# Kernel tuning notes

Measured on AMD Instinct MI355X. Metric: run time of the kernel, lower is better.

Reference implementation:

```python
import jax, jax.numpy as jnp
import numpy as np
from jax import lax

T, B = 32, 16
NUM_ACTIONS = 18
HID = 256
C_V, C_K, C_S, NQ = 120, 8, 64, 4
NKEY, NVAL = C_K + C_S, C_V + C_S
Hh, Ww = 27, 20


def _spatial_basis():
    # Fourier spatial basis from Mott et al.; U = V = 8 -> 64 channels.
    h, w, U = Hh, Ww, 8
    p_h = np.arange(1, h + 1)[:, None] * np.ones((1, w)) * (np.pi / h)
    p_w = np.ones((h, 1)) * np.arange(1, w + 1)[None, :] * (np.pi / w)
    u = np.arange(1, U + 1)
    a = np.cos(p_h[:, :, None] * u)  # (h,w,8)
    b = np.cos(p_w[:, :, None] * u)  # (h,w,8)
    S = np.einsum('hwu,hwv->hwuv', a, b).reshape(h, w, U * U)
    return jnp.asarray(S, jnp.float32)

_S = _spatial_basis()


def _conv(x, w, b, stride, pad):
    y = lax.conv_general_dilated(x, w, stride, pad,
                                 dimension_numbers=('NCHW', 'OIHW', 'NCHW'))
    return y + b[None, :, None, None]


def setup_inputs() -> dict:
    key = jax.random.key(0)
    ks = iter(jax.random.split(key, 40))
    f32 = jnp.float32
    def rn(shape, s=0.05):
        return jax.random.normal(next(ks), shape, dtype=f32) * s
    return dict(
        frame=jax.random.normal(next(ks), (T, B, 3, 210, 160), dtype=f32),
        done=jnp.zeros((T, B), dtype=bool),
        last_action=jax.random.randint(next(ks), (T, B), 0, NUM_ACTIONS),
        reward=jax.random.normal(next(ks), (T, B), dtype=f32),
        core_h=jnp.zeros((B, HID), f32), core_c=jnp.zeros((B, HID), f32),
        conv_h=jnp.zeros((B, HID // 2, Hh, Ww), f32),
        conv_c=jnp.zeros((B, HID // 2, Hh, Ww), f32),
        cnn_w1=rn((32, 3, 8, 8)), cnn_b1=rn((32,)),
        cnn_w2=rn((64, 32, 4, 4)), cnn_b2=rn((64,)),
        lstm_w=rn((512, 192, 3, 3)), lstm_b=rn((512,)),
        qw1=rn((HID, 128)), qb1=rn((128,)),
        qw2=rn((128, NQ * NKEY)), qb2=rn((NQ * NKEY,)),
        qw3=rn((NQ * NKEY, NQ * NKEY)), qb3=rn((NQ * NKEY,)),
        aw1=rn((NVAL * NQ + NKEY * NQ + 1 + NUM_ACTIONS, 2 * HID)), ab1=rn((2 * HID,)),
        aw2=rn((2 * HID, HID)), ab2=rn((HID,)),
        w_ih=rn((4 * HID, HID)), w_hh=rn((4 * HID, HID)),
        b_ih=rn((4 * HID,)), b_hh=rn((4 * HID,)),
        pw=rn((HID, NUM_ACTIONS)), pb=rn((NUM_ACTIONS,)),
        vw=rn((HID, 1)), vb=rn((1,)),
    )


def reference(frame, done, last_action, reward, core_h, core_c, conv_h, conv_c,
              cnn_w1, cnn_b1, cnn_w2, cnn_b2, lstm_w, lstm_b,
              qw1, qb1, qw2, qb2, qw3, qb3, aw1, ab1, aw2, ab2,
              w_ih, w_hh, b_ih, b_hh, pw, pb, vw, vb):
    x = frame.reshape(T * B, 3, 210, 160)
    x = _conv(x, cnn_w1, cnn_b1, (4, 4), [(1, 1), (2, 2)])
    x = _conv(x, cnn_w2, cnn_b2, (2, 2), [(2, 2), (1, 1)])  # (T*B,64,27,20)
    x = x.reshape(T, B, 64, Hh, Ww)
    nd = (~done).astype(jnp.float32)  # (T,B)

    def vis_step(carry, inp):
        h, c = carry
        x_t, nd_t = inp
        m = nd_t[:, None, None, None]
        h, c = m * h, m * c
        gates = _conv(jnp.concatenate([x_t, h], axis=1), lstm_w, lstm_b,
                      (1, 1), [(1, 1), (1, 1)])
        ai, af, ao, ag = jnp.split(gates, 4, axis=1)
        c = jax.nn.sigmoid(af) * c + jax.nn.sigmoid(ai) * jnp.tanh(ag)
        h = jax.nn.sigmoid(ao) * jnp.tanh(c)
        return (h, c), h

    (vh, vc), O = lax.scan(vis_step, (conv_h, conv_c), (x, nd))
    # Faithful to the original `.view(N, h, w, c)` (a reinterpret, not a transpose).
    O = O.reshape(T * B, Hh, Ww, 128)
    Sb = jnp.broadcast_to(_S, (T * B, Hh, Ww, C_S))
    K = jnp.concatenate([O[..., :C_K], Sb], axis=3).reshape(T, B, Hh, Ww, NKEY)
    V = jnp.concatenate([O[..., C_K:], Sb], axis=3).reshape(T, B, Hh, Ww, NVAL)

    a1h = jax.nn.one_hot(last_action, NUM_ACTIONS, dtype=jnp.float32)  # (T,B,A)
    r = jnp.clip(reward, -1.0, 1.0)[..., None]  # (T,B,1)

    def core_step(carry, inp):
        h, c = carry
        K_t, V_t, r_t, a_t, nd_t = inp
        q = jax.nn.relu(h @ qw1 + qb1)
        q = jax.nn.relu(q @ qw2 + qb2)
        q = (q @ qw3 + qb3).reshape(B, NQ, NKEY)
        A = jnp.einsum('bhwk,bqk->bhwq', K_t, q)
        A = jax.nn.softmax(A.reshape(B, Hh * Ww, NQ), axis=1).reshape(B, Hh, Ww, NQ)
        ans = jnp.einsum('bhwq,bhwv->bqv', A, V_t)  # (B,NQ,NVAL)
        answer = jnp.concatenate(
            [ans.reshape(B, -1), q.reshape(B, -1), r_t, a_t], axis=1)
        ci = jax.nn.relu(answer @ aw1 + ab1) @ aw2 + ab2
        m = nd_t[:, None]
        h, c = m * h, m * c
        gates = ci @ w_ih.T + b_ih + h @ w_hh.T + b_hh  # torch gate order i,f,g,o
        gi, gf, gg, go = jnp.split(gates, 4, axis=1)
        c = jax.nn.sigmoid(gf) * c + jax.nn.sigmoid(gi) * jnp.tanh(gg)
        h = jax.nn.sigmoid(go) * jnp.tanh(c)
        return (h, c), h

    (ch, cc), outs = lax.scan(core_step, (core_h, core_c), (K, V, r, a1h, nd))
    out = outs.reshape(T * B, HID)
    logits = out @ pw + pb
    values = out @ vw + vb
    action = jnp.argmax(logits, axis=1)  # eval-mode action selection
    return (logits.reshape(T, B, NUM_ACTIONS), values.reshape(T, B),
            action.reshape(T, B), ch, cc, vh, vc)
```

## Files before the change

### kernel.cpp

```cpp
#include <hip/hip_runtime.h>
#include <math.h>

#define T_ 32
#define B_ 16
#define NA 18
#define P_ 540

typedef __attribute__((ext_vector_type(8)))  short short8;
typedef __attribute__((ext_vector_type(16))) float f32x16;

__device__ __forceinline__ float sigm(float x){ return 1.0f/(1.0f+expf(-x)); }
__device__ __forceinline__ unsigned short f2bf(float f){
    unsigned u = __float_as_uint(f);
    u += 0x7fff + ((u>>16)&1u);
    return (unsigned short)(u>>16);
}
__device__ __forceinline__ float bfu(unsigned short u){ return __uint_as_float(((unsigned)u)<<16); }
__device__ __forceinline__ float BFLO(unsigned x){ return __uint_as_float(x<<16); }
__device__ __forceinline__ float BFHI(unsigned x){ return __uint_as_float(x & 0xffff0000u); }

__device__ __forceinline__ void conv1_block(const float* __restrict__ frame,
                                            const float* __restrict__ w,
                                            const float* __restrict__ bias,
                                            unsigned short* __restrict__ c1buf,
                                            int n, int slot, int oh, int tid, char* smraw){
    float* tile = (float*)smraw;
    const float* fb = frame + (size_t)n*3*210*160;
    for (int s = tid; s < 6048; s += 512){
        int col = s % 168;
        int row = (s/168) % 12;
        int ic  = s / 2016;
        int iy = oh*4 - 1 + row;
        int ix = col - 2;
        float v = 0.f;
        if (iy >= 0 && iy < 210 && ix >= 0 && ix < 160) v = fb[ic*33600 + iy*160 + ix];
        tile[s] = v;
    }
    __syncthreads();
    int oc = tid & 31, grp = (tid >> 5) & 7, rsel = tid >> 8;
    float acc[5] = {0.f,0.f,0.f,0.f,0.f};
    const float* wb = w + oc*192;
    for (int ic=0; ic<3; ++ic){
        #pragma unroll
        for (int kh=0; kh<8; ++kh){
            const float* wr = wb + ic*64 + kh*8;
            float4 w0 = *((const float4*)wr);
            float4 w1 = *((const float4*)(wr+4));
            const float* row = tile + ic*2016 + (kh + 4*rsel)*168 + grp*20;
            float r[24];
            *((float4*)(r+ 0)) = *((const float4*)(row+ 0));
            *((float4*)(r+ 4)) = *((const float4*)(row+ 4));
            *((float4*)(r+ 8)) = *((const float4*)(row+ 8));
            *((float4*)(r+12)) = *((const float4*)(row+12));
            *((float4*)(r+16)) = *((const float4*)(row+16));
            *((float4*)(r+20)) = *((const float4*)(row+20));
            #pragma unroll
            for (int o=0;o<5;++o){
                acc[o] += r[o*4+0]*w0.x + r[o*4+1]*w0.y + r[o*4+2]*w0.z + r[o*4+3]*w0.w
                        + r[o*4+4]*w1.x + r[o*4+5]*w1.y + r[o*4+6]*w1.z + r[o*4+7]*w1.w;
            }
        }
    }
    float bi = bias[oc];
    unsigned short* ob = c1buf + ((size_t)((slot*16 + (n & 15))*32 + oc)*56 + oh+2+rsel)*42 + 1;
    #pragma unroll
    for (int o=0;o<5;++o) ob[grp*5+o] = f2bf(acc[o] + bi);
}

__device__ __forceinline__ void c2_block(const unsigned short* __restrict__ c1buf,
                                         const unsigned short* __restrict__ apack2,
                                         const float* __restrict__ bias,
                                         unsigned short* __restrict__ xre,
                                         int s, int slot, int n0, int tid, char* smraw){
    unsigned short (*p2)[3072] = (unsigned short (*)[3072])smraw;
    float* bsm = (float*)(smraw + 12288);
    int wave = tid >> 6, lane = tid & 63;
    int khalf = (lane>>5) << 3;
    if (tid < 64) bsm[tid] = bias[tid];
    const unsigned short* cb = c1buf + (size_t)(slot*16 + (s & 15))*32*2352;

    int soff[4], swaddr[4];
    #pragma unroll
    for (int q=0;q<4;++q){
        int idx = q*512 + tid;
        int n = idx & 127, k = idx >> 7;
        int p = n0 + n; if (p > 539) p = 539;
        soff[q] = ((p/20)*2 + (k>>2))*42 + (p%20)*2 + (k&3);
        swaddr[q] = n*24 + k;
    }
    #pragma unroll
    for (int q=0;q<4;++q) p2[0][swaddr[q]] = cb[soff[q]];
    unsigned short rv[4];
    #pragma unroll
    for (int q=0;q<4;++q) rv[q] = cb[2352 + soff[q]];

    int mt = wave >> 2, nq = wave & 3;
    short8 acur = *((const short8*)(apack2 + ((size_t)mt*64 + lane)*8));
    short8 anxt;
    f32x16 acc;
    #pragma unroll
    for (int rg=0;rg<16;++rg) acc[rg] = 0.f;
    __syncthreads();

    for (int c=0; c<32; ++c){
        int buf = c & 1;
        if (c < 31){
            #pragma unroll
            for (int q=0;q<4;++q) p2[buf^1][swaddr[q]] = rv[q];
        }
        if (c < 30){
            const unsigned short* src = cb + (size_t)(c+2)*2352;
            #pragma unroll
            for (int q=0;q<4;++q) rv[q] = src[soff[q]];
        }
        if (c < 31) anxt = *((const short8*)(apack2 + ((size_t)((c+1)*2 + mt)*64 + lane)*8));
        {
            int n = nq*32 + (lane & 31);
            short8 bf = *((const short8*)(&p2[buf][n*24 + khalf]));
            acc = __builtin_amdgcn_mfma_f32_32x32x16_bf16(acur, bf, acc, 0, 0, 0);
        }
        acur = anxt;
        __syncthreads();
    }
    int pos = n0 + nq*32 + (lane & 31);
    if (pos < 540){
        unsigned short* op = xre + ((size_t)s*540 + pos)*64;
        #pragma unroll
        for (int rg=0; rg<16; ++rg){
            int oc = mt*32 + (rg & 3) + 8*(rg>>2) + 4*(lane>>5);
            op[oc] = f2bf(acc[rg] + bsm[oc]);
        }
    }
}

__global__ __launch_bounds__(512) void conv1pro(const float* __restrict__ frame,
                                                const float* __restrict__ w,
                                                const float* __restrict__ bias,
                                                unsigned short* __restrict__ c1buf){
    __shared__ __align__(16) char sm[24576];
    int n = blockIdx.x/26, oh = (blockIdx.x%26)*2;
    conv1_block(frame, w, bias, c1buf, n, (n>>4)%3, oh, threadIdx.x, sm);
}
__global__ __launch_bounds__(512) void c2pro(const unsigned short* __restrict__ c1buf,
                                             const unsigned short* __restrict__ apack2,
                                             const float* __restrict__ bias,
                                             unsigned short* __restrict__ xre){
    __shared__ __align__(16) char sm[12544];
    c2_block(c1buf, apack2, bias, xre, blockIdx.x/5, 0, (blockIdx.x%5)*128, threadIdx.x, sm);
}

__global__ void apack2k(const float* __restrict__ w2, unsigned short* __restrict__ ap){
    int idx = blockIdx.x*256 + threadIdx.x;
    if (idx >= 32768) return;
    int j = idx & 7;
    int lane = (idx>>3) & 63;
    int mt = (idx>>9) & 1;
    int ic = idx >> 10;
    int k = ((lane>>5)<<3) + j;
    int oc = mt*32 + (lane & 31);
    ap[idx] = f2bf(w2[((oc*32 + ic)<<4) + k]);
}

__global__ void sbasisk(float* __restrict__ S, float* __restrict__ ST){
    int idx = blockIdx.x*256 + threadIdx.x;
    if (idx >= P_*64) return;
    int s = idx & 63, p = idx >> 6;
    int y = p/20, x = p%20;
    int u = s >> 3, v = s & 7;
    double a  = cos((double)((y+1)*(u+1)) * M_PI / 27.0);
    double bb = cos((double)((x+1)*(v+1)) * M_PI / 20.0);
    float fv = (float)(a*bb);
    S[idx] = fv;
    ST[(size_t)s*540 + p] = fv;
}

__global__ void packw8k(const float* __restrict__ in, unsigned short* __restrict__ out, int R, int C){
    int idx = blockIdx.x*256 + threadIdx.x;
    int r8cnt = (R+7)>>3;
    if (idx >= r8cnt*C*8) return;
    int j = idx & 7;
    int rc = idx >> 3;
    int c = rc % C;
    int r = (rc / C)*8 + j;
    out[idx] = (r < R) ? f2bf(in[(size_t)r*C + c]) : (unsigned short)0;
}
__global__ void packt8k(const float* __restrict__ in, unsigned short* __restrict__ out, int R, int C){
    int idx = blockIdx.x*256 + threadIdx.x;
    int r8cnt = (R+7)>>3;
    if (idx >= r8cnt*C*8) return;
    int j = idx & 7;
    int rc = idx >> 3;
    int c = rc % C;
    int r = (rc / C)*8 + j;
    out[idx] = (r < R) ? f2bf(in[(size_t)c*R + r]) : (unsigned short)0;
}

__global__ void apack9k(const float* __restrict__ lw, unsigned short* __restrict__ ap){
    int idx = blockIdx.x*256 + threadIdx.x;
    if (idx >= 884736) return;
    int j = idx & 7;
    int lane = (idx>>3) & 63;
    int mt = (idx>>9) & 15;
    int f  = idx >> 13;
    int tap = f / 12, c = f % 12;
    int ch = c*16 + ((lane>>5)<<3) + j;
    int oc = mt*32 + (lane & 31);
    ap[idx] = f2bf(lw[(size_t)oc*1728 + ch*9 + tap]);
}

__global__ void h0rek(const float* __restrict__ h0, unsigned short* __restrict__ h0re){
    int idx = blockIdx.x*256 + threadIdx.x;
    if (idx >= 16*128*540) return;
    int plane = idx / 540, p = idx % 540;
    int b = plane >> 7, c = plane & 127;
    h0re[((size_t)b*540 + p)*128 + c] = f2bf(h0[idx]);
}

__global__ __launch_bounds__(512) void gvck(const float* __restrict__ frame,
                                            const float* __restrict__ cnn_w1,
                                            const float* __restrict__ cnn_b1,
                                            unsigned short* __restrict__ c1buf,
                                            const unsigned short* __restrict__ apack2,
                                            const float* __restrict__ cnn_b2,
                                            unsigned short* __restrict__ xre,
                                            const unsigned short* __restrict__ hrd,
                                            unsigned short* __restrict__ hwr,
                                            const unsigned short* __restrict__ h0re,
                                            const unsigned short* __restrict__ apack,
                                            const float* __restrict__ lb,
                                            const unsigned char* __restrict__ done,
                                            float* __restrict__ vh, float* __restrict__ vc,
                                            unsigned short* __restrict__ hreA,
                                            const float* __restrict__ S,
                                            const float* __restrict__ ST,
                                            const unsigned short* __restrict__ pq1, const float* __restrict__ qb1,
                                            const unsigned short* __restrict__ pq2, const float* __restrict__ qb2,
                                            const unsigned short* __restrict__ pq3, const float* __restrict__ qb3,
                                            const unsigned short* __restrict__ pa1, const float* __restrict__ ab1,
                                            const unsigned short* __restrict__ pa2, const float* __restrict__ ab2,
                                            const unsigned short* __restrict__ pih, const unsigned short* __restrict__ phh,
                                            const float* __restrict__ bih, const float* __restrict__ bhh,
                                            const float* __restrict__ reward, const int* __restrict__ lact,
                                            float* __restrict__ hsb, float* __restrict__ csb,
                                            float* __restrict__ outs,
                                            int t){
    __shared__ __align__(16) char smraw[65536];
    int bid = blockIdx.x;
    int tid = threadIdx.x;

    if (bid >= 720){
        int tp1 = t + 1; if (tp1 > 31) return;
        int idx = bid - 720;
        c2_block(c1buf, apack2, cnn_b2, xre, tp1*16 + idx/5, tp1%3, (idx%5)*128, tid, smraw);
        return;
    }
    if (bid >= 304){
        int tp2 = t + 2; if (tp2 > 31) return;
        int idx = bid - 304;
        conv1_block(frame, cnn_w1, cnn_b1, c1buf, tp2*16 + idx/26, tp2%3, (idx%26)*2, tid, smraw);
        return;
    }

    if (bid >= 16){
        if (t >= T_) return;
        float* gsm = (float*)smraw;
        int vb = bid - 16;
        int b  = vb % 16;
        int r  = vb / 16;
        int nb = r % 9;
        int mh = r / 9;
        int wave = tid >> 6, lane = tid & 63;
        int khalf = (lane>>5) << 3;
        int n0 = nb * 64;
        bool dn = done[t*B_ + b];

        const unsigned short* xb = xre + (size_t)(t*B_ + b)*540*64;
        const unsigned short* hp2 = (t==0) ? (h0re + (size_t)b*540*128)
                                           : (hrd  + (size_t)b*540*128);

        int mt = (wave>>1)*4 + mh*2 + (wave&1);

        int poff[2][9]; int vmask[2][9];
        #pragma unroll
        for (int jj=0;jj<2;++jj){
            int p = n0 + jj*32 + (lane & 31); if (p > 539) p = 539;
            int y = p/20, x = p%20;
            #pragma unroll
            for (int tap=0;tap<9;++tap){
                int dy = tap/3 - 1, dx = tap%3 - 1;
                int yy = y+dy, xx = x+dx;
                vmask[jj][tap] = ((unsigned)yy < 27u) && ((unsigned)xx < 20u);
                poff[jj][tap] = yy*20 + xx;
            }
        }
        const short8 z8 = {0,0,0,0,0,0,0,0};
        f32x16 acc[2];
        #pragma unroll
        for (int jj=0;jj<2;++jj)
            #pragma unroll
            for (int rg=0;rg<16;++rg) acc[jj][rg] = 0.f;

        for (int c=0;c<4;++c){
            int cho = c*16 + khalf;
            #pragma unroll
            for (int tap=0;tap<9;++tap){
                short8 af = *((const short8*)(apack + ((size_t)((tap*12+c)*16 + mt)*64 + lane)*8));
                short8 b0 = vmask[0][tap] ? *((const short8*)(xb + poff[0][tap]*64 + cho)) : z8;
                short8 b1 = vmask[1][tap] ? *((const short8*)(xb + poff[1][tap]*64 + cho)) : z8;
                acc[0] = __builtin_amdgcn_mfma_f32_32x32x16_bf16(af, b0, acc[0], 0, 0, 0);
                acc[1] = __builtin_amdgcn_mfma_f32_32x32x16_bf16(af, b1, acc[1], 0, 0, 0);
            }
        }
        if (!dn){
            for (int c=4;c<12;++c){
                int cho = (c-4)*16 + khalf;
                #pragma unroll
                for (int tap=0;tap<9;++tap){
                    short8 af = *((const short8*)(apack + ((size_t)((tap*12+c)*16 + mt)*64 + lane)*8));
                    short8 b0 = vmask[0][tap] ? *((const short8*)(hp2 + poff[0][tap]*128 + cho)) : z8;
                    short8 b1 = vmask[1][tap] ? *((const short8*)(hp2 + poff[1][tap]*128 + cho)) : z8;
                    acc[0] = __builtin_amdgcn_mfma_f32_32x32x16_bf16(af, b0, acc[0], 0, 0, 0);
                    acc[1] = __builtin_amdgcn_mfma_f32_32x32x16_bf16(af, b1, acc[1], 0, 0, 0);
                }
            }
        }

        int g8 = wave >> 1, ih = wave & 1;
        #pragma unroll
        for (int j=0;j<2;++j){
            int p_loc = j*32 + (lane & 31);
            #pragma unroll
            for (int rg=0; rg<16; ++rg){
                int c_loc = ih*32 + 4*(lane>>5) + (rg & 3) + 8*(rg>>2);
                gsm[g8*4096 + c_loc*64 + p_loc] = acc[j][rg];
            }
        }
        __syncthreads();

        {
            int p_loc = tid & 63, c0 = tid >> 6;
            int pg = n0 + p_loc;
            if (pg < 540){
                float m = dn ? 0.f : 1.f;
                #pragma unroll
                for (int e=0;e<8;++e){
                    int c_loc = c0*8 + e;
                    int cg = mh*64 + c_loc;
                    float gi = gsm[        c_loc*64 + p_loc] + lb[      cg];
                    float gf = gsm[ 4096 + c_loc*64 + p_loc] + lb[128 + cg];
                    float go = gsm[ 8192 + c_loc*64 + p_loc] + lb[256 + cg];
                    float gg = gsm[12288 + c_loc*64 + p_loc] + lb[384 + cg];
                    size_t idx = ((size_t)b*128 + cg)*540 + pg;
                    float cold = vc[idx] * m;
                    float cn = sigm(gf)*cold + sigm(gi)*tanhf(gg);
                    float hn = sigm(go)*tanhf(cn);
                    vc[idx] = cn;
                    if (t == T_-1) vh[idx] = hn;
                    unsigned short hb16 = f2bf(hn);
                    hwr[((size_t)b*540 + pg)*128 + cg] = hb16;
                    int flat = cg*540 + pg;
                    int pos = (flat/2560)*20 + (flat/128)%20;
                    int ch  = flat & 127;
                    hreA[((size_t)(t*B_ + b)*540 + pos)*128 + ch] = hb16;
                }
            }
        }
        return;
    }

    if (t == 0) return;
    int tc = t - 1;
    int b = bid;
    float* fs = (float*)smraw;
    float* hs   = fs;
    float* cs   = fs + 256;
    float* hs2  = fs + 512;
    float* q1   = fs + 768;
    float* q2   = fs + 896;
    float* q3   = fs + 1184;
    float* elog = fs + 1472;
    float* red  = fs + 3632;
    float* ansv = fs + 3664;
    float* hid  = fs + 4720;
    float* cis  = fs + 5232;
    float* gb   = fs + 5488;

    if (tid < 256){ hs[tid] = hsb[b*256+tid]; cs[tid] = csb[b*256+tid]; }
    if (tid >= 256 && tid < 269) ansv[1043 + (tid-256)] = 0.f;
    __syncthreads();

    float m = done[tc*B_+b] ? 0.f : 1.f;
    if (tid < 128){
        float a0=0.f,a1=0.f,a2=0.f,a3=0.f;
        for (int i8=0;i8<32;++i8){
            uint4 w = *((const uint4*)(pq1 + ((size_t)(i8<<7)+tid)*8));
            float4 ha = *((const float4*)(hs + i8*8));
            float4 hb2 = *((const float4*)(hs + i8*8 + 4));
            a0 += ha.x*BFLO(w.x);  a1 += ha.y*BFHI(w.x);
            a2 += ha.z*BFLO(w.y);  a3 += ha.w*BFHI(w.y);
            a0 += hb2.x*BFLO(w.z); a1 += hb2.y*BFHI(w.z);
            a2 += hb2.z*BFLO(w.w); a3 += hb2.w*BFHI(w.w);
        }
        q1[tid] = fmaxf(qb1[tid] + ((a0+a1)+(a2+a3)), 0.f);
    }
    __syncthreads();
    if (tid < 288){
        float a0=0.f,a1=0.f,a2=0.f,a3=0.f;
        for (int i8=0;i8<16;++i8){
            uint4 w = *((const uint4*)(pq2 + ((size_t)i8*288+tid)*8));
            float4 ha = *((const float4*)(q1 + i8*8));
            float4 hb2 = *((const float4*)(q1 + i8*8 + 4));
            a0 += ha.x*BFLO(w.x);  a1 += ha.y*BFHI(w.x);
            a2 += ha.z*BFLO(w.y);  a3 += ha.w*BFHI(w.y);
            a0 += hb2.x*BFLO(w.z); a1 += hb2.y*BFHI(w.z);
            a2 += hb2.z*BFLO(w.w); a3 += hb2.w*BFHI(w.w);
        }
        q2[tid] = fmaxf(qb2[tid] + ((a0+a1)+(a2+a3)), 0.f);
    }
    __syncthreads();
    if (tid < 288){
        float a0=0.f,a1=0.f,a2=0.f,a3=0.f;
        for (int i8=0;i8<36;++i8){
            uint4 w = *((const uint4*)(pq3 + ((size_t)i8*288+tid)*8));
            float4 ha = *((const float4*)(q2 + i8*8));
            float4 hb2 = *((const float4*)(q2 + i8*8 + 4));
            a0 += ha.x*BFLO(w.x);  a1 += ha.y*BFHI(w.x);
            a2 += ha.z*BFLO(w.y);  a3 += ha.w*BFHI(w.y);
            a0 += hb2.x*BFLO(w.z); a1 += hb2.y*BFHI(w.z);
            a2 += hb2.z*BFLO(w.w); a3 += hb2.w*BFHI(w.w);
        }
        float a = qb3[tid] + ((a0+a1)+(a2+a3));
        q3[tid] = a;
        ansv[736+tid] = a;
    }
    if (tid == 0){ float r = reward[tc*B_+b]; ansv[1024] = fminf(1.f,fmaxf(-1.f,r)); }
    if (tid >= 32 && tid < 32+NA) ansv[1025 + tid-32] = (lact[tc*B_+b] == tid-32) ? 1.f : 0.f;
    __syncthreads();

    const unsigned short* hrb = hreA + (size_t)(tc*B_ + b)*540*128;
    for (int idx = tid; idx < 4*P_; idx += 512){
        int qi = idx / P_, p = idx % P_;
        const unsigned short* hp = hrb + (size_t)p*128;
        uint4 hv = *((const uint4*)hp);
        const float* qv = q3 + qi*72;
        float a = BFLO(hv.x)*qv[0] + BFHI(hv.x)*qv[1]
                + BFLO(hv.y)*qv[2] + BFHI(hv.y)*qv[3]
                + BFLO(hv.z)*qv[4] + BFHI(hv.z)*qv[5]
                + BFLO(hv.w)*qv[6] + BFHI(hv.w)*qv[7];
        const float* Sp = S + p*64;
        #pragma unroll
        for (int s2=0;s2<16;++s2){
            float4 sv = *((const float4*)(Sp + 4*s2));
            a += sv.x*qv[8+4*s2] + sv.y*qv[9+4*s2] + sv.z*qv[10+4*s2] + sv.w*qv[11+4*s2];
        }
        elog[qi*P_ + p] = a;
    }
    __syncthreads();
    {
        int qi = tid >> 7, lt = tid & 127;
        float mx = -1e30f;
        for (int p = lt; p < P_; p += 128) mx = fmaxf(mx, elog[qi*P_ + p]);
        for (int off=32; off; off>>=1) mx = fmaxf(mx, __shfl_down(mx, off));
        if ((tid & 63) == 0) red[tid>>6] = mx;
        __syncthreads();
        if (tid < 4) red[16+tid] = fmaxf(red[2*tid], red[2*tid+1]);
        __syncthreads();
        mx = red[16+qi];
        float sm = 0.f;
        for (int p = lt; p < P_; p += 128){ float e = expf(elog[qi*P_ + p]-mx); elog[qi*P_ + p] = e; sm += e; }
        for (int off=32; off; off>>=1) sm += __shfl_down(sm, off);
        if ((tid & 63) == 0) red[8 + (tid>>6)] = sm;
        __syncthreads();
        if (tid < 4) red[24+tid] = red[8+2*tid] + red[8+2*tid+1];
        __syncthreads();
    }
    if (tid < 480){
        int g = tid >> 3;
        int qi = g / 15, vb = g % 15;
        int pc = tid & 7;
        float ac[8] = {0,0,0,0,0,0,0,0};
        const unsigned short* hb8 = hrb + 8 + vb*8;
        for (int p = pc; p < P_; p += 8){
            float e = elog[qi*P_ + p];
            uint4 hv = *((const uint4*)(hb8 + (size_t)p*128));
            ac[0] += e*BFLO(hv.x); ac[1] += e*BFHI(hv.x);
            ac[2] += e*BFLO(hv.y); ac[3] += e*BFHI(hv.y);
            ac[4] += e*BFLO(hv.z); ac[5] += e*BFHI(hv.z);
            ac[6] += e*BFLO(hv.w); ac[7] += e*BFHI(hv.w);
        }
        #pragma unroll
        for (int j=0;j<8;++j){ ac[j] += __shfl_down(ac[j],4); ac[j] += __shfl_down(ac[j],2); ac[j] += __shfl_down(ac[j],1); }
        if (pc == 0){
            float inv2 = 1.f/red[24+qi];
            #pragma unroll
            for (int j=0;j<8;++j) ansv[qi*184 + vb*8 + j] = ac[j]*inv2;
        }
    }
    {
        int g = tid >> 3;
        int qi = g >> 4, vb4 = g & 15;
        int pc = tid & 7;
        float s0=0.f, s1=0.f, s2v=0.f, s3=0.f;
        const float* S0 = ST + (size_t)(vb4*4)*540;
        for (int p = pc; p < P_; p += 8){
            float e = elog[qi*P_ + p];
            s0 += e*S0[p]; s1 += e*S0[540+p]; s2v += e*S0[1080+p]; s3 += e*S0[1620+p];
        }
        s0 += __shfl_down(s0,4); s0 += __shfl_down(s0,2); s0 += __shfl_down(s0,1);
        s1 += __shfl_down(s1,4); s1 += __shfl_down(s1,2); s1 += __shfl_down(s1,1);
        s2v += __shfl_down(s2v,4); s2v += __shfl_down(s2v,2); s2v += __shfl_down(s2v,1);
        s3 += __shfl_down(s3,4); s3 += __shfl_down(s3,2); s3 += __shfl_down(s3,1);
        if (pc == 0){
            float inv2 = 1.f/red[24+qi];
            ansv[qi*184 + 120 + vb4*4 + 0] = s0*inv2;
            ansv[qi*184 + 120 + vb4*4 + 1] = s1*inv2;
            ansv[qi*184 + 120 + vb4*4 + 2] = s2v*inv2;
            ansv[qi*184 + 120 + vb4*4 + 3] = s3*inv2;
        }
    }
    __syncthreads();
    {
        float a0=ab1[tid], a1=0.f, a2=0.f, a3=0.f;
        for (int i8=0;i8<131;++i8){
            uint4 w = *((const uint4*)(pa1 + ((size_t)(i8<<9)+tid)*8));
            float4 av = *((const float4*)(ansv + i8*8));
            float4 av2 = *((const float4*)(ansv + i8*8 + 4));
            a0 += av.x*BFLO(w.x);  a1 += av.y*BFHI(w.x);
            a2 += av.z*BFLO(w.y);  a3 += av.w*BFHI(w.y);
            a0 += av2.x*BFLO(w.z); a1 += av2.y*BFHI(w.z);
            a2 += av2.z*BFLO(w.w); a3 += av2.w*BFHI(w.w);
        }
        hid[tid] = fmaxf((a0+a1)+(a2+a3), 0.f);
    }
    if (tid < 256) hs2[tid] = hs[tid]*m;
    __syncthreads();
    if (tid < 256){
        float a0=ab2[tid],a1=0.f,a2=0.f,a3=0.f;
        for (int i8=0;i8<64;++i8){
            uint4 w = *((const uint4*)(pa2 + ((size_t)(i8<<8)+tid)*8));
            float4 hv = *((const float4*)(hid + i8*8));
            float4 hv2 = *((const float4*)(hid + i8*8 + 4));
            a0 += hv.x*BFLO(w.x);  a1 += hv.y*BFHI(w.x);
            a2 += hv.z*BFLO(w.y);  a3 += hv.w*BFHI(w.y);
            a0 += hv2.x*BFLO(w.z); a1 += hv2.y*BFHI(w.z);
            a2 += hv2.z*BFLO(w.w); a3 += hv2.w*BFHI(w.w);
        }
        cis[tid] = (a0+a1)+(a2+a3);
    }
    __syncthreads();
    for (int g = tid; g < 1024; g += 512){
        float a0=bih[g]+bhh[g], a1=0.f, a2=0.f, a3=0.f;
        for (int i8=0;i8<32;++i8){
            uint4 wi = *((const uint4*)(pih + ((size_t)(i8<<10)+g)*8));
            uint4 wh = *((const uint4*)(phh + ((size_t)(i8<<10)+g)*8));
            float4 ca = *((const float4*)(cis + i8*8));
            float4 cb2 = *((const float4*)(cis + i8*8 + 4));
            float4 ha = *((const float4*)(hs2 + i8*8));
            float4 hb2 = *((const float4*)(hs2 + i8*8 + 4));
            a0 += ca.x*BFLO(wi.x) + ha.x*BFLO(wh.x);
            a1 += ca.y*BFHI(wi.x) + ha.y*BFHI(wh.x);
            a2 += ca.z*BFLO(wi.y) + ha.z*BFLO(wh.y);
            a3 += ca.w*BFHI(wi.y) + ha.w*BFHI(wh.y);
            a0 += cb2.x*BFLO(wi.z) + hb2.x*BFLO(wh.z);
            a1 += cb2.y*BFHI(wi.z) + hb2.y*BFHI(wh.z);
            a2 += cb2.z*BFLO(wi.w) + hb2.z*BFLO(wh.w);
            a3 += cb2.w*BFHI(wi.w) + hb2.w*BFHI(wh.w);
        }
        gb[g] = (a0+a1)+(a2+a3);
    }
    __syncthreads();
    if (tid < 256){
        float gi = gb[tid], gf = gb[256+tid], gg = gb[512+tid], go = gb[768+tid];
        float cold = cs[tid]*m;
        float cn = sigm(gf)*cold + sigm(gi)*tanhf(gg);
        float hn = sigm(go)*tanhf(cn);
        csb[b*256+tid] = cn;
        hsb[b*256+tid] = hn;
        outs[(tc*B_+b)*256+tid] = hn;
    }
}

__global__ __launch_bounds__(64) void finalk(const float* __restrict__ outs,
                                             const float* __restrict__ pw, const float* __restrict__ pb,
                                             const float* __restrict__ vw, const float* __restrict__ vb,
                                             float* __restrict__ dout){
    int row = blockIdx.x, tid = threadIdx.x;
    __shared__ float os[256];
    __shared__ float lg[NA];
    for (int i=tid; i<256; i+=64) os[i] = outs[row*256+i];
    __syncthreads();
    if (tid < NA){
        float a = pb[tid];
        for (int i=0;i<256;++i) a += os[i]*pw[i*NA+tid];
        lg[tid] = a;
        dout[row*NA + tid] = a;
    } else if (tid == 32){
        float a = vb[0];
        for (int i=0;i<256;++i) a += os[i]*vw[i];
        dout[9216 + row] = a;
    }
    __syncthreads();
    if (tid == 0){
        int am = 0; float bv = lg[0];
        for (int j=1;j<NA;++j) if (lg[j] > bv){ bv = lg[j]; am = j; }
        dout[9728 + row] = (float)am;
    }
}

extern "C" void kernel_launch(void* const* d_in, const int* in_sizes, int n_in,
                              void* d_out, int out_size, void* d_ws, size_t ws_size,
                              hipStream_t stream) {
    const float* frame   = (const float*)d_in[0];
    const unsigned char* done = (const unsigned char*)d_in[1];
    const int*   lact    = (const int*)d_in[2];
    const float* reward  = (const float*)d_in[3];
    const float* core_h0 = (const float*)d_in[4];
    const float* core_c0 = (const float*)d_in[5];
    const float* conv_h0 = (const float*)d_in[6];
    const float* conv_c0 = (const float*)d_in[7];
    const float* cnn_w1  = (const float*)d_in[8];
    const float* cnn_b1  = (const float*)d_in[9];
    const float* cnn_w2  = (const float*)d_in[10];
    const float* cnn_b2  = (const float*)d_in[11];
    const float* lstm_w  = (const float*)d_in[12];
    const float* lstm_b  = (const float*)d_in[13];
    const float* qw1 = (const float*)d_in[14]; const float* qb1 = (const float*)d_in[15];
    const float* qw2 = (const float*)d_in[16]; const float* qb2 = (const float*)d_in[17];
    const float* qw3 = (const float*)d_in[18]; const float* qb3 = (const float*)d_in[19];
    const float* aw1 = (const float*)d_in[20]; const float* ab1 = (const float*)d_in[21];
    const float* aw2 = (const float*)d_in[22]; const float* ab2 = (const float*)d_in[23];
    const float* w_ih = (const float*)d_in[24]; const float* w_hh = (const float*)d_in[25];
    const float* b_ih = (const float*)d_in[26]; const float* b_hh = (const float*)d_in[27];
    const float* pw = (const float*)d_in[28]; const float* pb = (const float*)d_in[29];
    const float* vw = (const float*)d_in[30]; const float* vb = (const float*)d_in[31];

    float* ws = (float*)d_ws;
    float* dout = (float*)d_out;

    unsigned short* xre    = (unsigned short*)ws;
    unsigned short* hreA   = (unsigned short*)(ws + 10485760);
    unsigned short* apack  = (unsigned short*)(ws + 28180480);
    unsigned short* wpk    = (unsigned short*)(ws + 28966912);
    unsigned short* pq1 = wpk;
    unsigned short* pq2 = wpk + 32768;
    unsigned short* pq3 = wpk + 69632;
    unsigned short* pa1 = wpk + 152576;
    unsigned short* pa2 = wpk + 689152;
    unsigned short* pih = wpk + 820224;
    unsigned short* phh = wpk + 1082368;
    unsigned short* h0re   = (unsigned short*)(ws + 29753344);
    unsigned short* apack2 = (unsigned short*)(ws + 30408704);
    unsigned short* hpl0   = (unsigned short*)(ws + 30425088);
    float* hsb   = ws + 31080448;
    float* csb   = ws + 31084544;
    unsigned short* hpl1   = (unsigned short*)(ws + 31100928);
    unsigned short* c1buf  = (unsigned short*)(ws + 31653888);
    float* ST    = ws + 33460224;
    float* vh    = ws + 34881536;
    float* vc    = ws + 35987456;
    float* S     = ws + 37093376;
    float* outs  = ws + 37127936;

    hipMemsetAsync(c1buf, 0, (size_t)3612672*2, stream);

    apack2k<<<128, 256, 0, stream>>>(cnn_w2, apack2);
    sbasisk<<<135, 256, 0, stream>>>(S, ST);
    apack9k<<<3456, 256, 0, stream>>>(lstm_w, apack);
    packw8k<<<128,  256, 0, stream>>>(qw1, pq1, 256, 128);
    packw8k<<<144,  256, 0, stream>>>(qw2, pq2, 128, 288);
    packw8k<<<324,  256, 0, stream>>>(qw3, pq3, 288, 288);
    packw8k<<<2096, 256, 0, stream>>>(aw1, pa1, 1043, 512);
    packw8k<<<512,  256, 0, stream>>>(aw2, pa2, 512, 256);
    packt8k<<<1024, 256, 0, stream>>>(w_ih, pih, 256, 1024);
    packt8k<<<1024, 256, 0, stream>>>(w_hh, phh, 256, 1024);
    h0rek<<<4320, 256, 0, stream>>>(conv_h0, h0re);
    hipMemcpyAsync(vc,  conv_c0, (size_t)16*128*540*sizeof(float), hipMemcpyDeviceToDevice, stream);
    hipMemcpyAsync(hsb, core_h0, (size_t)16*256*sizeof(float), hipMemcpyDeviceToDevice, stream);
    hipMemcpyAsync(csb, core_c0, (size_t)16*256*sizeof(float), hipMemcpyDeviceToDevice, stream);

    conv1pro<<<832, 512, 0, stream>>>(frame, cnn_w1, cnn_b1, c1buf);
    c2pro<<<80, 512, 0, stream>>>(c1buf, apack2, cnn_b2, xre);

    for (int t = 0; t <= T_; ++t){
        gvck<<<800, 512, 0, stream>>>(frame, cnn_w1, cnn_b1, c1buf, apack2, cnn_b2, xre,
                                      (t&1)?hpl0:hpl1, (t&1)?hpl1:hpl0, h0re,
                                      apack, lstm_b, done, vh, vc, hreA,
                                      S, ST, pq1,qb1,pq2,qb2,pq3,qb3,
                                      pa1,ab1,pa2,ab2, pih,phh,b_ih,b_hh,
                                      reward, lact, hsb, csb, outs, t);
    }

    finalk<<<512, 64, 0, stream>>>(outs, pw, pb, vw, vb, dout);

    hipMemcpyAsync(dout + 10240,   outs + (size_t)31*B_*256, (size_t)16*256*sizeof(float), hipMemcpyDeviceToDevice, stream);
    hipMemcpyAsync(dout + 14336,   csb, (size_t)16*256*sizeof(float), hipMemcpyDeviceToDevice, stream);
    hipMemcpyAsync(dout + 18432,   vh,  (size_t)16*128*540*sizeof(float), hipMemcpyDeviceToDevice, stream);
    hipMemcpyAsync(dout + 1124352, vc,  (size_t)16*128*540*sizeof(float), hipMemcpyDeviceToDevice, stream);
}
```

Before: 5.349 ms.

## Hoist CNN convs out of recurrent loop into batched upfront kernels

Undoes the software pipelining that computed conv1 and conv2 for future timesteps inside each recurrent step kernel. Instead, conv1 and conv2 run once over all 512 frames before the time loop, writing into a full-size padded buffer. The recurrent kernel now launches only the 304 blocks needed for the ConvLSTM and core work. It also retiles conv1 and conv2 to 256-thread blocks with more output per thread. The full-size padded buffer aliases hreA and needs a much larger memset, which adds traffic and relies on hreA being written only after c2mfma has finished.

```diff
diff --git a/kernel.cpp b/kernel.cpp
--- a/kernel.cpp
+++ b/kernel.cpp
@@ -19,14 +19,16 @@
 __device__ __forceinline__ float BFLO(unsigned x){ return __uint_as_float(x<<16); }
 __device__ __forceinline__ float BFHI(unsigned x){ return __uint_as_float(x & 0xffff0000u); }
 
-__device__ __forceinline__ void conv1_block(const float* __restrict__ frame,
-                                            const float* __restrict__ w,
-                                            const float* __restrict__ bias,
-                                            unsigned short* __restrict__ c1buf,
-                                            int n, int slot, int oh, int tid, char* smraw){
-    float* tile = (float*)smraw;
+__global__ __launch_bounds__(256) void conv1k(const float* __restrict__ frame,
+                                              const float* __restrict__ w,
+                                              const float* __restrict__ bias,
+                                              unsigned short* __restrict__ c1pad){
+    __shared__ float tile[6048];
+    int bid = blockIdx.x;
+    int n = bid / 26, oh = (bid % 26)*2;
+    int tid = threadIdx.x;
     const float* fb = frame + (size_t)n*3*210*160;
-    for (int s = tid; s < 6048; s += 512){
+    for (int s = tid; s < 6048; s += 256){
         int col = s % 168;
         int row = (s/168) % 12;
         int ic  = s / 2016;
@@ -37,8 +39,8 @@
         tile[s] = v;
     }
     __syncthreads();
-    int oc = tid & 31, grp = (tid >> 5) & 7, rsel = tid >> 8;
-    float acc[5] = {0.f,0.f,0.f,0.f,0.f};
+    int oc = tid & 31, grp = tid >> 5;
+    float acc[10] = {0.f,0.f,0.f,0.f,0.f,0.f,0.f,0.f,0.f,0.f};
     const float* wb = w + oc*192;
     for (int ic=0; ic<3; ++ic){
         #pragma unroll
@@ -46,107 +48,40 @@
             const float* wr = wb + ic*64 + kh*8;
             float4 w0 = *((const float4*)wr);
             float4 w1 = *((const float4*)(wr+4));
-            const float* row = tile + ic*2016 + (kh + 4*rsel)*168 + grp*20;
+            const float* rowA = tile + ic*2016 + kh*168 + grp*20;
             float r[24];
-            *((float4*)(r+ 0)) = *((const float4*)(row+ 0));
-            *((float4*)(r+ 4)) = *((const float4*)(row+ 4));
-            *((float4*)(r+ 8)) = *((const float4*)(row+ 8));
-            *((float4*)(r+12)) = *((const float4*)(row+12));
-            *((float4*)(r+16)) = *((const float4*)(row+16));
-            *((float4*)(r+20)) = *((const float4*)(row+20));
+            *((float4*)(r+ 0)) = *((const float4*)(rowA+ 0));
+            *((float4*)(r+ 4)) = *((const float4*)(rowA+ 4));
+            *((float4*)(r+ 8)) = *((const float4*)(rowA+ 8));
+            *((float4*)(r+12)) = *((const float4*)(rowA+12));
+            *((float4*)(r+16)) = *((const float4*)(rowA+16));
+            *((float4*)(r+20)) = *((const float4*)(rowA+20));
             #pragma unroll
             for (int o=0;o<5;++o){
                 acc[o] += r[o*4+0]*w0.x + r[o*4+1]*w0.y + r[o*4+2]*w0.z + r[o*4+3]*w0.w
                         + r[o*4+4]*w1.x + r[o*4+5]*w1.y + r[o*4+6]*w1.z + r[o*4+7]*w1.w;
             }
+            const float* rowB = rowA + 672;
+            *((float4*)(r+ 0)) = *((const float4*)(rowB+ 0));
+            *((float4*)(r+ 4)) = *((const float4*)(rowB+ 4));
+            *((float4*)(r+ 8)) = *((const float4*)(rowB+ 8));
+            *((float4*)(r+12)) = *((const float4*)(rowB+12));
+            *((float4*)(r+16)) = *((const float4*)(rowB+16));
+            *((float4*)(r+20)) = *((const float4*)(rowB+20));
+            #pragma unroll
+            for (int o=0;o<5;++o){
+                acc[5+o] += r[o*4+0]*w0.x + r[o*4+1]*w0.y + r[o*4+2]*w0.z + r[o*4+3]*w0.w
+                          + r[o*4+4]*w1.x + r[o*4+5]*w1.y + r[o*4+6]*w1.z + r[o*4+7]*w1.w;
+            }
         }
     }
     float bi = bias[oc];
-    unsigned short* ob = c1buf + ((size_t)((slot*16 + (n & 15))*32 + oc)*56 + oh+2+rsel)*42 + 1;
+    unsigned short* ob = c1pad + ((size_t)(n*32 + oc)*56 + oh+2)*42 + 1;
     #pragma unroll
     for (int o=0;o<5;++o) ob[grp*5+o] = f2bf(acc[o] + bi);
-}
-
-__device__ __forceinline__ void c2_block(const unsigned short* __restrict__ c1buf,
-                                         const unsigned short* __restrict__ apack2,
-                                         const float* __restrict__ bias,
-                                         unsigned short* __restrict__ xre,
-                                         int s, int slot, int n0, int tid, char* smraw){
-    unsigned short (*p2)[3072] = (unsigned short (*)[3072])smraw;
-    float* bsm = (float*)(smraw + 12288);
-    int wave = tid >> 6, lane = tid & 63;
-    int khalf = (lane>>5) << 3;
-    if (tid < 64) bsm[tid] = bias[tid];
-    const unsigned short* cb = c1buf + (size_t)(slot*16 + (s & 15))*32*2352;
-
-    int soff[4], swaddr[4];
+    ob += 42;
     #pragma unroll
-    for (int q=0;q<4;++q){
-        int idx = q*512 + tid;
-        int n = idx & 127, k = idx >> 7;
-        int p = n0 + n; if (p > 539) p = 539;
-        soff[q] = ((p/20)*2 + (k>>2))*42 + (p%20)*2 + (k&3);
-        swaddr[q] = n*24 + k;
-    }
-    #pragma unroll
-    for (int q=0;q<4;++q) p2[0][swaddr[q]] = cb[soff[q]];
-    unsigned short rv[4];
-    #pragma unroll
-    for (int q=0;q<4;++q) rv[q] = cb[2352 + soff[q]];
-
-    int mt = wave >> 2, nq = wave & 3;
-    short8 acur = *((const short8*)(apack2 + ((size_t)mt*64 + lane)*8));
-    short8 anxt;
-    f32x16 acc;
-    #pragma unroll
-    for (int rg=0;rg<16;++rg) acc[rg] = 0.f;
-    __syncthreads();
-
-    for (int c=0; c<32; ++c){
-        int buf = c & 1;
-        if (c < 31){
-            #pragma unroll
-            for (int q=0;q<4;++q) p2[buf^1][swaddr[q]] = rv[q];
-        }
-        if (c < 30){
-            const unsigned short* src = cb + (size_t)(c+2)*2352;
-            #pragma unroll
-            for (int q=0;q<4;++q) rv[q] = src[soff[q]];
-        }
-        if (c < 31) anxt = *((const short8*)(apack2 + ((size_t)((c+1)*2 + mt)*64 + lane)*8));
-        {
-            int n = nq*32 + (lane & 31);
-            short8 bf = *((const short8*)(&p2[buf][n*24 + khalf]));
-            acc = __builtin_amdgcn_mfma_f32_32x32x16_bf16(acur, bf, acc, 0, 0, 0);
-        }
-        acur = anxt;
-        __syncthreads();
-    }
-    int pos = n0 + nq*32 + (lane & 31);
-    if (pos < 540){
-        unsigned short* op = xre + ((size_t)s*540 + pos)*64;
-        #pragma unroll
-        for (int rg=0; rg<16; ++rg){
-            int oc = mt*32 + (rg & 3) + 8*(rg>>2) + 4*(lane>>5);
-            op[oc] = f2bf(acc[rg] + bsm[oc]);
-        }
-    }
-}
-
-__global__ __launch_bounds__(512) void conv1pro(const float* __restrict__ frame,
-                                                const float* __restrict__ w,
-                                                const float* __restrict__ bias,
-                                                unsigned short* __restrict__ c1buf){
-    __shared__ __align__(16) char sm[24576];
-    int n = blockIdx.x/26, oh = (blockIdx.x%26)*2;
-    conv1_block(frame, w, bias, c1buf, n, (n>>4)%3, oh, threadIdx.x, sm);
-}
-__global__ __launch_bounds__(512) void c2pro(const unsigned short* __restrict__ c1buf,
-                                             const unsigned short* __restrict__ apack2,
-                                             const float* __restrict__ bias,
-                                             unsigned short* __restrict__ xre){
-    __shared__ __align__(16) char sm[12544];
-    c2_block(c1buf, apack2, bias, xre, blockIdx.x/5, 0, (blockIdx.x%5)*128, threadIdx.x, sm);
+    for (int o=0;o<5;++o) ob[grp*5+o] = f2bf(acc[5+o] + bi);
 }
 
 __global__ void apack2k(const float* __restrict__ w2, unsigned short* __restrict__ ap){
@@ -159,6 +94,80 @@
     int k = ((lane>>5)<<3) + j;
     int oc = mt*32 + (lane & 31);
     ap[idx] = f2bf(w2[((oc*32 + ic)<<4) + k]);
+}
+
+__global__ __launch_bounds__(256) void c2mfma(const unsigned short* __restrict__ c1pad,
+                                              const unsigned short* __restrict__ apack2,
+                                              const float* __restrict__ bias,
+                                              unsigned short* __restrict__ xre){
+    __shared__ unsigned short p2[2][3072];
+    __shared__ float bsm[64];
+    int bid = blockIdx.x;
+    int s = bid / 5;
+    int n0 = (bid % 5) * 128;
+    int tid = threadIdx.x;
+    int wave = tid >> 6, lane = tid & 63;
+    int khalf = (lane>>5) << 3;
+    if (tid < 64) bsm[tid] = bias[tid];
+    const unsigned short* cb = c1pad + (size_t)s*32*2352;
+
+    int soff[8], swaddr[8];
+    #pragma unroll
+    for (int q=0;q<8;++q){
+        int idx = q*256 + tid;
+        int n = idx & 127, k = idx >> 7;
+        int p = n0 + n; if (p > 539) p = 539;
+        soff[q] = ((p/20)*2 + (k>>2))*42 + (p%20)*2 + (k&3);
+        swaddr[q] = n*24 + k;
+    }
+    #pragma unroll
+    for (int q=0;q<8;++q) p2[0][swaddr[q]] = cb[soff[q]];
+    unsigned short rv[8];
+    #pragma unroll
+    for (int q=0;q<8;++q) rv[q] = cb[2352 + soff[q]];
+
+    int mt = wave >> 1, ntb = (wave & 1) * 2;
+    short8 acur = *((const short8*)(apack2 + ((size_t)mt*64 + lane)*8));
+    short8 anxt;
+    f32x16 acc[2];
+    #pragma unroll
+    for (int jj=0;jj<2;++jj)
+        #pragma unroll
+        for (int rg=0;rg<16;++rg) acc[jj][rg] = 0.f;
+    __syncthreads();
+
+    for (int c=0; c<32; ++c){
+        int buf = c & 1;
+        if (c < 31){
+            #pragma unroll
+            for (int q=0;q<8;++q) p2[buf^1][swaddr[q]] = rv[q];
+        }
+        if (c < 30){
+            const unsigned short* src = cb + (size_t)(c+2)*2352;
+            #pragma unroll
+            for (int q=0;q<8;++q) rv[q] = src[soff[q]];
+        }
+        if (c < 31) anxt = *((const short8*)(apack2 + ((size_t)((c+1)*2 + mt)*64 + lane)*8));
+        #pragma unroll
+        for (int jj=0;jj<2;++jj){
+            int n = (ntb+jj)*32 + (lane & 31);
+            short8 bf = *((const short8*)(&p2[buf][n*24 + khalf]));
+            acc[jj] = __builtin_amdgcn_mfma_f32_32x32x16_bf16(acur, bf, acc[jj], 0, 0, 0);
+        }
+        acur = anxt;
+        __syncthreads();
+    }
+    #pragma unroll
+    for (int jj=0;jj<2;++jj){
+        int pos = n0 + (ntb+jj)*32 + (lane & 31);
+        if (pos >= 540) continue;
+        unsigned short* op = xre + ((size_t)s*540 + pos)*64;
+        #pragma unroll
+        for (int rg=0; rg<16; ++rg){
+            int oc = mt*32 + (rg & 3) + 8*(rg>>2) + 4*(lane>>5);
+            op[oc] = f2bf(acc[jj][rg] + bsm[oc]);
+        }
+    }
 }
 
 __global__ void sbasisk(float* __restrict__ S, float* __restrict__ ST){
@@ -216,13 +225,7 @@
     h0re[((size_t)b*540 + p)*128 + c] = f2bf(h0[idx]);
 }
 
-__global__ __launch_bounds__(512) void gvck(const float* __restrict__ frame,
-                                            const float* __restrict__ cnn_w1,
-                                            const float* __restrict__ cnn_b1,
-                                            unsigned short* __restrict__ c1buf,
-                                            const unsigned short* __restrict__ apack2,
-                                            const float* __restrict__ cnn_b2,
-                                            unsigned short* __restrict__ xre,
+__global__ __launch_bounds__(512) void gvpk(const unsigned short* __restrict__ xre,
                                             const unsigned short* __restrict__ hrd,
                                             unsigned short* __restrict__ hwr,
                                             const unsigned short* __restrict__ h0re,
@@ -247,19 +250,6 @@
     __shared__ __align__(16) char smraw[65536];
     int bid = blockIdx.x;
     int tid = threadIdx.x;
-
-    if (bid >= 720){
-        int tp1 = t + 1; if (tp1 > 31) return;
-        int idx = bid - 720;
-        c2_block(c1buf, apack2, cnn_b2, xre, tp1*16 + idx/5, tp1%3, (idx%5)*128, tid, smraw);
-        return;
-    }
-    if (bid >= 304){
-        int tp2 = t + 2; if (tp2 > 31) return;
-        int idx = bid - 304;
-        conv1_block(frame, cnn_w1, cnn_b1, c1buf, tp2*16 + idx/26, tp2%3, (idx%26)*2, tid, smraw);
-        return;
-    }
 
     if (bid >= 16){
         if (t >= T_) return;
@@ -638,6 +628,7 @@
     float* dout = (float*)d_out;
 
     unsigned short* xre    = (unsigned short*)ws;
+    unsigned short* c1pad  = (unsigned short*)(ws + 10485760);
     unsigned short* hreA   = (unsigned short*)(ws + 10485760);
     unsigned short* apack  = (unsigned short*)(ws + 28180480);
     unsigned short* wpk    = (unsigned short*)(ws + 28966912);
@@ -654,16 +645,18 @@
     float* hsb   = ws + 31080448;
     float* csb   = ws + 31084544;
     unsigned short* hpl1   = (unsigned short*)(ws + 31100928);
-    unsigned short* c1buf  = (unsigned short*)(ws + 31653888);
     float* ST    = ws + 33460224;
     float* vh    = ws + 34881536;
     float* vc    = ws + 35987456;
     float* S     = ws + 37093376;
     float* outs  = ws + 37127936;
 
-    hipMemsetAsync(c1buf, 0, (size_t)3612672*2, stream);
+    hipMemsetAsync(c1pad, 0, (size_t)38535168*2, stream);
 
     apack2k<<<128, 256, 0, stream>>>(cnn_w2, apack2);
+    conv1k<<<512*26, 256, 0, stream>>>(frame, cnn_w1, cnn_b1, c1pad);
+    c2mfma<<<2560, 256, 0, stream>>>(c1pad, apack2, cnn_b2, xre);
+
     sbasisk<<<135, 256, 0, stream>>>(S, ST);
     apack9k<<<3456, 256, 0, stream>>>(lstm_w, apack);
     packw8k<<<128,  256, 0, stream>>>(qw1, pq1, 256, 128);
@@ -678,11 +671,8 @@
     hipMemcpyAsync(hsb, core_h0, (size_t)16*256*sizeof(float), hipMemcpyDeviceToDevice, stream);
     hipMemcpyAsync(csb, core_c0, (size_t)16*256*sizeof(float), hipMemcpyDeviceToDevice, stream);
 
-    conv1pro<<<832, 512, 0, stream>>>(frame, cnn_w1, cnn_b1, c1buf);
-    c2pro<<<80, 512, 0, stream>>>(c1buf, apack2, cnn_b2, xre);
-
     for (int t = 0; t <= T_; ++t){
-        gvck<<<800, 512, 0, stream>>>(frame, cnn_w1, cnn_b1, c1buf, apack2, cnn_b2, xre,
+        gvpk<<<304, 512, 0, stream>>>(xre,
                                       (t&1)?hpl0:hpl1, (t&1)?hpl1:hpl0, h0re,
                                       apack, lstm_b, done, vh, vc, hreA,
                                       S, ST, pq1,qb1,pq2,qb2,pq3,qb3,
```

New measurement: 4.723 ms. 1.13x faster.
